# Performance work log

Measured on AMD Instinct MI355X. Metric: run time of the kernel, lower is better.

Reference implementation:

```python
import jax, jax.numpy as jnp
import numpy as np

D_IN = 2048
D_OUT = 2048
H = 16
QK_ROPE = 64
QK_NOPE = 64
QK_HEAD = QK_NOPE + QK_ROPE  # 128
V_HEAD = 128
KV_RANK = 512
THETA = 10000.0
EPS = 1e-6


def rms_norm(x, w):
    var = jnp.mean(x * x, axis=-1, keepdims=True)
    return x * jax.lax.rsqrt(var + EPS) * w


def apply_rope(x, theta=THETA):
    # x: [B, S, H, D] with D even; interleaved-pair rotation (torchtune style)
    B, S, NH, D = x.shape
    half = D // 2
    freqs = 1.0 / (theta ** (jnp.arange(0, D, 2, dtype=jnp.float32) / D))  # [D/2]
    ang = jnp.arange(S, dtype=jnp.float32)[:, None] * freqs[None, :]       # [S, D/2]
    cos = jnp.cos(ang)[None, :, None, :]  # [1,S,1,D/2]
    sin = jnp.sin(ang)[None, :, None, :]
    xp = x.reshape(B, S, NH, half, 2)
    x1, x2 = xp[..., 0], xp[..., 1]
    out = jnp.stack([x1 * cos - x2 * sin, x2 * cos + x1 * sin], axis=-1)
    return out.reshape(B, S, NH, D).astype(x.dtype)


def setup_inputs() -> dict:
    key = jax.random.key(0)
    ks = jax.random.split(key, 6)
    B, S = 2, 2048
    s = lambda fan_in: 1.0 / np.sqrt(fan_in)
    x = jax.random.normal(ks[0], (B, S, D_IN), dtype=jnp.float32)
    w_query = jax.random.uniform(ks[1], (D_IN, H * QK_HEAD), jnp.float32, -s(D_IN), s(D_IN))
    wkv_a = jax.random.uniform(ks[2], (D_IN, KV_RANK + QK_ROPE), jnp.float32, -s(D_IN), s(D_IN))
    wkv_b = jax.random.uniform(ks[3], (KV_RANK, H * (QK_NOPE + V_HEAD)), jnp.float32, -s(KV_RANK), s(KV_RANK))
    kv_norm_w = jnp.ones((KV_RANK,), jnp.float32)
    out_proj_w = jax.random.uniform(ks[4], (H * V_HEAD, D_OUT), jnp.float32, -s(H * V_HEAD), s(H * V_HEAD))
    return {"x": x, "w_query": w_query, "wkv_a": wkv_a, "wkv_b": wkv_b,
            "kv_norm_w": kv_norm_w, "out_proj_w": out_proj_w}


def reference(x, w_query, wkv_a, wkv_b, kv_norm_w, out_proj_w):
    B, S, _ = x.shape
    scale = QK_HEAD ** -0.5
    # queries (no q-lora)
    q = (x @ w_query).reshape(B, S, H, QK_HEAD)
    # low-rank KV compression
    kv = x @ wkv_a                                    # [B,S,KV_RANK+QK_ROPE]
    kv_c, k_pe = kv[..., :KV_RANK], kv[..., KV_RANK:]
    kv_dec = (rms_norm(kv_c, kv_norm_w) @ wkv_b).reshape(B, S, H, QK_NOPE + V_HEAD)
    k_nope, v = kv_dec[..., :QK_NOPE], kv_dec[..., QK_NOPE:]
    k_pe = jnp.broadcast_to(k_pe[:, :, None, :], (B, S, H, QK_ROPE))
    q_nope, q_pe = q[..., :QK_NOPE], q[..., QK_NOPE:]
    q_pe = apply_rope(q_pe)
    k_pe = apply_rope(k_pe)
    queries = jnp.concatenate([q_nope, q_pe], axis=-1)   # [B,S,H,QK_HEAD]
    keys = jnp.concatenate([k_nope, k_pe], axis=-1)
    # attention
    scores = jnp.einsum('bqhd,bkhd->bhqk', queries, keys) * scale
    mask = jnp.triu(jnp.ones((S, S), dtype=bool), k=1)
    scores = jnp.where(mask[None, None], -jnp.inf, scores)
    attn = jax.nn.softmax(scores.astype(jnp.float32), axis=-1).astype(x.dtype)
    out = jnp.einsum('bhqk,bkhd->bqhd', attn, v).reshape(B, S, H * V_HEAD)
    return out @ out_proj_w
```

## Files before the change

### kernel.cpp

```cpp
#include <hip/hip_runtime.h>
#include <hip/hip_bf16.h>
#include <math.h>

#define BATCH   2
#define SEQ     2048
#define D_IN    2048
#define NHEAD   16
#define QK_ROPE 64
#define QK_NOPE 64
#define QK_HEAD 128
#define V_HEAD  128
#define KV_RANK 512
#define KV_W    640
#define NTOK    (BATCH*SEQ)
#define EPS_F   1e-6f

typedef unsigned short u16;
typedef short bf16x8 __attribute__((ext_vector_type(8)));
typedef float f32x4  __attribute__((ext_vector_type(4)));

__device__ __forceinline__ u16 f2bf(float f) {
    unsigned u = __float_as_uint(f);
    return (u16)((u + 0x7fffu + ((u >> 16) & 1u)) >> 16);
}
__device__ __forceinline__ float bf2f(u16 u) {
    return __uint_as_float(((unsigned)u) << 16);
}
__device__ __forceinline__ float exp2_hw(float x) {
    float r;
    asm volatile("v_exp_f32 %0, %1\n\ts_nop 0" : "=v"(r) : "v"(x));
    return r;
}
__device__ __forceinline__ void gload16(const void* g, void* l) {
    __builtin_amdgcn_global_load_lds((const __attribute__((address_space(1))) unsigned int*)g,
                                     (__attribute__((address_space(3))) unsigned int*)l, 16, 0, 0);
}

__device__ __forceinline__ void transpose_sec(const float* __restrict__ src,
                                              u16* __restrict__ dst,
                                              int N, int K, int bx, int by,
                                              float (*tile)[33], int tid) {
    const int tx = tid & 31, ty = tid >> 5;
    const int nb = bx * 32, kb = by * 32;
#pragma unroll
    for (int i = 0; i < 4; ++i) {
        int k = kb + ty + 8 * i, n = nb + tx;
        tile[ty + 8 * i][tx] = (n < N) ? src[(size_t)k * N + n] : 0.f;
    }
    __syncthreads();
#pragma unroll
    for (int i = 0; i < 4; ++i) {
        int n = nb + ty + 8 * i, k = kb + tx;
        dst[(size_t)n * K + k] = f2bf(tile[tx][ty + 8 * i]);
    }
}

__global__ __launch_bounds__(256) void prep(const float* __restrict__ x, u16* __restrict__ x_bf,
                                            const float* __restrict__ wq, u16* __restrict__ wqT,
                                            const float* __restrict__ wkva, u16* __restrict__ wkvaT,
                                            const float* __restrict__ wkvb, u16* __restrict__ wkvbT,
                                            const float* __restrict__ op, u16* __restrict__ opT,
                                            float* __restrict__ tab) {
    __shared__ float tile[32][33];
    const int idx = blockIdx.x;
    const int tid = threadIdx.x;
    if (idx < 8192) {
        int gid = idx * 256 + tid;
        float4 v = ((const float4*)x)[gid];
        unsigned lo = (unsigned)f2bf(v.x) | ((unsigned)f2bf(v.y) << 16);
        unsigned hi = (unsigned)f2bf(v.z) | ((unsigned)f2bf(v.w) << 16);
        ((uint2*)x_bf)[gid] = make_uint2(lo, hi);
    } else if (idx < 12288) {
        int s = idx - 8192;
        transpose_sec(wq, wqT, 2048, 2048, s % 64, s / 64, tile, tid);
    } else if (idx < 13568) {
        int s = idx - 12288;
        transpose_sec(wkva, wkvaT, 576, 2048, s % 20, s / 20, tile, tid);
    } else if (idx < 15104) {
        int s = idx - 13568;
        transpose_sec(wkvb, wkvbT, 3072, 512, s % 96, s / 96, tile, tid);
    } else if (idx < 19200) {
        int s = idx - 15104;
        transpose_sec(op, opT, 2048, 2048, s % 64, s / 64, tile, tid);
    } else {
        int gid = (idx - 19200) * 256 + tid;
        int i = gid & 31, s = gid >> 5;
        float freq = __expf(-(float)(2 * i) / 64.0f * 9.210340371976184f);
        float ang = (float)s * freq;
        tab[2 * gid]     = cosf(ang);
        tab[2 * gid + 1] = sinf(ang);
    }
}

template <int EPI>
__global__ __launch_bounds__(512, 1) void gemm256(const u16* __restrict__ A,
                                                  const u16* __restrict__ BT,
                                                  void* __restrict__ out0,
                                                  void* __restrict__ out1,
                                                  const float* __restrict__ tab,
                                                  int gx, int N, int K, float oscale) {
    __shared__ u16 lds[49152];
    const int tid = threadIdx.x;
    const int w = tid >> 6, l = tid & 63;
    const int lr = l & 15, lg = l >> 4;
    const int wr = w >> 2;
    const int wc = w & 3;
    const int nwg = gridDim.x, q8 = nwg >> 3;
    const int wg = (blockIdx.x & 7) * q8 + (blockIdx.x >> 3);
    const int row0 = (wg / gx) * 256, col0 = (wg % gx) * 256;
    const int NT = K >> 5;

    f32x4 acc[8][4];
#pragma unroll
    for (int m = 0; m < 8; ++m)
#pragma unroll
        for (int n = 0; n < 4; ++n) acc[m][n] = (f32x4){0.f, 0.f, 0.f, 0.f};

    auto stageA = [&](int bufi, int kt) {
        u16* base = lds + bufi * 8192;
        const u16* g = A + (size_t)row0 * K + kt * 32;
#pragma unroll
        for (int i = 0; i < 2; ++i) {
            int L = (i * 512 + tid) * 16;
            int s = L ^ (((L >> 6) & 3) << 4);
            gload16(g + (size_t)(L >> 6) * K + ((s & 63) >> 1), base + (L >> 1));
        }
    };
    auto stageB = [&](int bufi, int kt) {
        u16* base = lds + 24576 + bufi * 8192;
        const u16* g = BT + (size_t)col0 * K + kt * 32;
#pragma unroll
        for (int i = 0; i < 2; ++i) {
            int L = (i * 512 + tid) * 16;
            int s = L ^ (((L >> 6) & 3) << 4);
            gload16(g + (size_t)(L >> 6) * K + ((s & 63) >> 1), base + (L >> 1));
        }
    };

    stageA(0, 0); stageB(0, 0); stageA(1, 1); stageB(1, 1);

    for (int t = 0; t < NT; ++t) {
        const int buf = t % 3, nb2 = (t + 2) % 3;
        u16* Ab = lds + buf * 8192;
        u16* Bb = lds + 24576 + buf * 8192;
        if (t + 1 < NT) asm volatile("s_waitcnt vmcnt(4)" ::: "memory");
        else            asm volatile("s_waitcnt vmcnt(0)" ::: "memory");
        __builtin_amdgcn_s_barrier();
        __builtin_amdgcn_sched_barrier(0);

        bf16x8 bfg[4], af[4];
#pragma unroll
        for (int n = 0; n < 4; ++n) {
            int row = wc * 64 + n * 16 + lr;
            bfg[n] = *(const bf16x8*)&Bb[row * 32 + (((lg * 16) ^ ((row & 3) << 4)) >> 1)];
        }
#pragma unroll
        for (int i = 0; i < 4; ++i) {
            int row = wr * 128 + i * 16 + lr;
            af[i] = *(const bf16x8*)&Ab[row * 32 + (((lg * 16) ^ ((row & 3) << 4)) >> 1)];
        }
        if (t + 2 < NT) stageA(nb2, t + 2);
        __builtin_amdgcn_s_barrier();
        asm volatile("s_waitcnt lgkmcnt(0)" ::: "memory");
        __builtin_amdgcn_sched_barrier(0);
        __builtin_amdgcn_s_setprio(1);
#pragma unroll
        for (int i = 0; i < 4; ++i)
#pragma unroll
            for (int n = 0; n < 4; ++n)
                acc[i][n] = __builtin_amdgcn_mfma_f32_16x16x32_bf16(af[i], bfg[n], acc[i][n], 0, 0, 0);
        __builtin_amdgcn_s_setprio(0);

#pragma unroll
        for (int i = 0; i < 4; ++i) {
            int row = wr * 128 + (4 + i) * 16 + lr;
            af[i] = *(const bf16x8*)&Ab[row * 32 + (((lg * 16) ^ ((row & 3) << 4)) >> 1)];
        }
        if (t + 2 < NT) stageB(nb2, t + 2);
        __builtin_amdgcn_s_barrier();
        asm volatile("s_waitcnt lgkmcnt(0)" ::: "memory");
        __builtin_amdgcn_sched_barrier(0);
        __builtin_amdgcn_s_setprio(1);
#pragma unroll
        for (int i = 0; i < 4; ++i)
#pragma unroll
            for (int n = 0; n < 4; ++n)
                acc[4 + i][n] = __builtin_amdgcn_mfma_f32_16x16x32_bf16(af[i], bfg[n], acc[4 + i][n], 0, 0, 0);
        __builtin_amdgcn_s_setprio(0);
    }

    if (EPI == 0) {
        u16* qp = (u16*)out0;
        float* kvp = (float*)out1;
        const bool pe = (wc & 1);
#pragma unroll
        for (int m = 0; m < 8; ++m)
#pragma unroll
            for (int n = 0; n < 4; ++n) {
                int c = col0 + wc * 64 + n * 16 + lr;
#pragma unroll
                for (int j = 0; j < 4; ++j) {
                    int r = row0 + wr * 128 + m * 16 + 4 * lg + j;
                    float v = acc[m][n][j];
                    if (c < 2048) {
                        v *= oscale;
                        if (pe) {
                            int s = r & (SEQ - 1);
                            int ip = (16 * n + lr) >> 1;
                            float2 cs = ((const float2*)tab)[s * 32 + ip];
                            float part = __shfl_xor(v, 1);
                            v = (lr & 1) ? (v * cs.x + part * cs.y)
                                         : (v * cs.x - part * cs.y);
                        }
                        qp[(size_t)r * 2048 + c] = f2bf(v);
                    } else if (c < 2688) {
                        kvp[(size_t)r * KV_W + (c - 2048)] = v;
                    }
                }
            }
    } else {
        u16* Kall = (u16*)out0;
        u16* Vt   = (u16*)out1;
#pragma unroll
        for (int m = 0; m < 8; ++m) {
            int r0 = row0 + wr * 128 + m * 16 + 4 * lg;
            int b  = r0 >> 11;
            int s0 = r0 & (SEQ - 1);
#pragma unroll
            for (int n = 0; n < 4; ++n) {
                int c = col0 + wc * 64 + n * 16 + lr;
                int h = (unsigned)c / 192u;
                int cr = c - h * 192;
                int bh = b * NHEAD + h;
                if (cr < 64) {
#pragma unroll
                    for (int j = 0; j < 4; ++j) {
                        int s = s0 + j;
                        Kall[((size_t)bh * SEQ + s) * 128 + (cr ^ ((s & 7) << 3))] = f2bf(acc[m][n][j]);
                    }
                } else {
                    int d = cr - 64;
                    union { u16 u[4]; uint2 v; } pk;
#pragma unroll
                    for (int j = 0; j < 4; ++j) pk.u[j] = f2bf(acc[m][n][j]);
                    size_t base = ((size_t)bh * 128 + d) * SEQ + (s0 & ~63);
                    *(uint2*)&Vt[base + ((s0 & 63) ^ ((d & 7) << 3))] = pk.v;
                }
            }
        }
    }
}

__global__ __launch_bounds__(512, 1) void gemm_out(const u16* __restrict__ A,
                                                   const u16* __restrict__ BT,
                                                   float* __restrict__ C,
                                                   int N, int K) {
    __shared__ u16 lds[73728];
    const int tid = threadIdx.x;
    const int w = tid >> 6, l = tid & 63;
    const int lr = l & 15, lg = l >> 4;
    const int wr = w >> 1, wc = w & 1;
    const int nwg = gridDim.x, q8 = nwg >> 3;
    const int wg = (blockIdx.x & 7) * q8 + (blockIdx.x >> 3);
    const int gx = N >> 7;
    const int row0 = (wg / gx) * 256, col0 = (wg % gx) * 128;
    const int NT = K >> 6;

    f32x4 acc[4][4];
#pragma unroll
    for (int m = 0; m < 4; ++m)
#pragma unroll
        for (int n = 0; n < 4; ++n) acc[m][n] = (f32x4){0.f, 0.f, 0.f, 0.f};

    auto stageA = [&](int bufi, int h, int kt) {
        u16* base = lds + bufi * 16384 + h * 8192;
        const u16* g = A + (size_t)(row0 + h * 128) * K + kt * 64;
#pragma unroll
        for (int i = 0; i < 2; ++i) {
            int L = (i * 512 + tid) * 16;
            int s = L ^ (((L >> 7) & 7) << 4);
            gload16(g + (size_t)(s >> 7) * K + ((s & 127) >> 1), base + (L >> 1));
        }
    };
    auto stageB = [&](int bufi, int kt) {
        u16* base = lds + 49152 + bufi * 8192;
        const u16* g = BT + (size_t)col0 * K + kt * 64;
#pragma unroll
        for (int i = 0; i < 2; ++i) {
            int L = (i * 512 + tid) * 16;
            int s = L ^ (((L >> 7) & 7) << 4);
            gload16(g + (size_t)(s >> 7) * K + ((s & 127) >> 1), base + (L >> 1));
        }
    };

    stageA(0, 0, 0); stageA(0, 1, 0); stageB(0, 0);
    stageA(1, 0, 1); stageA(1, 1, 1); stageB(1, 1);

    const int ar0 = (wr & 1) * 64;

    for (int t = 0; t < NT; ++t) {
        const int buf = t % 3, nb2 = (t + 2) % 3;
        u16* Ab = lds + buf * 16384 + (wr >> 1) * 8192;
        u16* Bb = lds + 49152 + buf * 8192;
        if (t + 1 < NT) asm volatile("s_waitcnt vmcnt(6)" ::: "memory");
        else            asm volatile("s_waitcnt vmcnt(0)" ::: "memory");
        __builtin_amdgcn_s_barrier();
        __builtin_amdgcn_sched_barrier(0);

#pragma unroll
        for (int q = 0; q < 2; ++q) {
            bf16x8 af[4], bfg[4];
#pragma unroll
            for (int i = 0; i < 4; ++i) {
                int row = ar0 + i * 16 + lr;
                int byte = row * 128 + q * 64 + lg * 16;
                af[i] = *(const bf16x8*)&Ab[(byte ^ ((row & 7) << 4)) >> 1];
            }
#pragma unroll
            for (int n = 0; n < 4; ++n) {
                int row = wc * 64 + n * 16 + lr;
                int byte = row * 128 + q * 64 + lg * 16;
                bfg[n] = *(const bf16x8*)&Bb[(byte ^ ((row & 7) << 4)) >> 1];
            }
            if (t + 2 < NT) {
                if (q == 0) { stageA(nb2, 0, t + 2); stageA(nb2, 1, t + 2); }
                else        { stageB(nb2, t + 2); }
            }
            __builtin_amdgcn_s_barrier();
            asm volatile("s_waitcnt lgkmcnt(0)" ::: "memory");
            __builtin_amdgcn_sched_barrier(0);
            __builtin_amdgcn_s_setprio(1);
#pragma unroll
            for (int i = 0; i < 4; ++i)
#pragma unroll
                for (int n = 0; n < 4; ++n)
                    acc[i][n] = __builtin_amdgcn_mfma_f32_16x16x32_bf16(
                        af[i], bfg[n], acc[i][n], 0, 0, 0);
            __builtin_amdgcn_s_setprio(0);
        }
    }

#pragma unroll
    for (int m = 0; m < 4; ++m)
#pragma unroll
        for (int n = 0; n < 4; ++n) {
            int c = col0 + wc * 64 + n * 16 + lr;
#pragma unroll
            for (int j = 0; j < 4; ++j) {
                int r = row0 + wr * 64 + m * 16 + 4 * lg + j;
                C[(size_t)r * N + c] = acc[m][n][j];
            }
        }
}

__global__ __launch_bounds__(256) void rmsnorm_bf(const float* __restrict__ kv,
                                                  const float* __restrict__ w,
                                                  u16* __restrict__ c_norm,
                                                  const float* __restrict__ tab,
                                                  u16* __restrict__ K_all) {
    __shared__ float red[256];
    const int row = blockIdx.x, t = threadIdx.x;
    const float* src = kv + (size_t)row * KV_W;
    float v0 = src[t], v1 = src[t + 256];
    red[t] = v0 * v0 + v1 * v1;
    __syncthreads();
    for (int s = 128; s > 0; s >>= 1) {
        if (t < s) red[t] += red[t + s];
        __syncthreads();
    }
    const float inv = rsqrtf(red[0] / (float)KV_RANK + EPS_F);
    u16* dst = c_norm + (size_t)row * KV_RANK;
    dst[t]       = f2bf(v0 * inv * w[t]);
    dst[t + 256] = f2bf(v1 * inv * w[t + 256]);

    if (t < 16) {
        const int dq = t;
        const int s = row & (SEQ - 1);
        const int b = row >> 11;
        float4 v = *(const float4*)(src + KV_RANK + 4 * dq);
        const int i0 = 2 * dq;
        float2 cs0 = ((const float2*)tab)[s * 32 + i0];
        float2 cs1 = ((const float2*)tab)[s * 32 + i0 + 1];
        union { u16 u[4]; uint2 w2; } pk;
        pk.u[0] = f2bf(v.x * cs0.x - v.y * cs0.y);
        pk.u[1] = f2bf(v.y * cs0.x + v.x * cs0.y);
        pk.u[2] = f2bf(v.z * cs1.x - v.w * cs1.y);
        pk.u[3] = f2bf(v.w * cs1.x + v.z * cs1.y);
        const int idx = (64 + 4 * dq) ^ ((s & 7) << 3);
#pragma unroll
        for (int h = 0; h < NHEAD; ++h) {
            int bh = b * NHEAD + h;
            *(uint2*)&K_all[((size_t)bh * SEQ + s) * 128 + idx] = pk.w2;
        }
    }
}

#define QTILE 64
#define KTILE 64

__global__ __launch_bounds__(256, 2) void attn_mfma(const u16* __restrict__ q_bf,
                                                    const u16* __restrict__ K_all,
                                                    const u16* __restrict__ Vt,
                                                    u16* __restrict__ attn_bf) {
    __shared__ u16 Kbuf[2][KTILE * 128];
    __shared__ u16 Vbuf[2][128 * KTILE];
    __shared__ u16 Plds[4][16 * KTILE];

    const int idx = blockIdx.x;
    const int bh = (idx & 7) + 8 * (idx >> 7);
    const int pi = (idx >> 3) & 15;
    const int b = bh >> 4, h = bh & 15;

    const int tid = threadIdx.x;
    const int w = tid >> 6, l = tid & 63;
    const int lr = l & 15, lg = l >> 4;
    const u16* Kb = K_all + (size_t)bh * SEQ * 128;
    const u16* Vb = Vt + (size_t)bh * 128 * SEQ;
    const int sw = (lr & 7) << 3;
    u16* pw = Plds[w];

    auto stage = [&](int bufi, int k0) {
        u16* kb = Kbuf[bufi];
        u16* vb = Vbuf[bufi];
#pragma unroll
        for (int it = 0; it < 4; ++it) {
            int ci = it * 256 + tid;
            gload16(Kb + (((size_t)(k0 + (ci >> 4))) << 7) + ((ci & 15) << 3),
                    kb + (ci << 3));
        }
#pragma unroll
        for (int it = 0; it < 4; ++it) {
            int ci = it * 256 + tid;
            gload16(Vb + (size_t)(ci >> 3) * SEQ + k0 + ((ci & 7) << 3),
                    vb + (ci << 3));
        }
    };

    const int qbA = (31 - pi) * QTILE;
    const int qbB = pi * QTILE;

    stage(0, 0);
    int cur = 0;
    for (int half = 0; half < 2; ++half) {
        const int qbase = half ? qbB : qbA;
        const int nkt = (qbase >> 6) + 1;
        const int qg = qbase + 16 * w + lr;

        const u16* qrow = q_bf + (size_t)(b * SEQ + qg) * 2048 + h * QK_HEAD;
        bf16x8 qf[4];
#pragma unroll
        for (int dc = 0; dc < 4; ++dc) qf[dc] = *(const bf16x8*)(qrow + dc * 32 + lg * 8);

        f32x4 oacc[8];
#pragma unroll
        for (int ft = 0; ft < 8; ++ft) oacc[ft] = (f32x4){0.f, 0.f, 0.f, 0.f};
        float m_r = -1e30f, l_r = 0.f;

        for (int kt = 0; kt < nkt; ++kt) {
            const int k0 = kt * KTILE;
            if (kt + 1 < nkt) {
                stage(cur ^ 1, k0 + KTILE);
                asm volatile("s_waitcnt vmcnt(8)" ::: "memory");
            } else if (half == 0) {
                stage(cur ^ 1, 0);
                asm volatile("s_waitcnt vmcnt(8)" ::: "memory");
            } else {
                asm volatile("s_waitcnt vmcnt(0)" ::: "memory");
            }
            __builtin_amdgcn_s_barrier();
            __builtin_amdgcn_sched_barrier(0);

            const u16* kb = Kbuf[cur];
            const u16* vb = Vbuf[cur];

            f32x4 s[4];
            __builtin_amdgcn_s_setprio(1);
#pragma unroll
            for (int f = 0; f < 4; ++f) {
                s[f] = (f32x4){0.f, 0.f, 0.f, 0.f};
#pragma unroll
                for (int dc = 0; dc < 4; ++dc) {
                    bf16x8 kf = *(const bf16x8*)&kb[(16 * f + lr) * 128 + ((32 * dc + 8 * lg) ^ sw)];
                    s[f] = __builtin_amdgcn_mfma_f32_16x16x32_bf16(kf, qf[dc], s[f], 0, 0, 0);
                }
            }
            __builtin_amdgcn_s_setprio(0);

            if (kt == nkt - 1) {
#pragma unroll
                for (int f = 0; f < 4; ++f)
#pragma unroll
                    for (int j = 0; j < 4; ++j)
                        if (k0 + 16 * f + 4 * lg + j > qg) s[f][j] = -1e30f;
            }

            float t0 = fmaxf(fmaxf(s[0][0], s[0][1]), fmaxf(s[0][2], s[0][3]));
            float t1 = fmaxf(fmaxf(s[1][0], s[1][1]), fmaxf(s[1][2], s[1][3]));
            float t2 = fmaxf(fmaxf(s[2][0], s[2][1]), fmaxf(s[2][2], s[2][3]));
            float t3 = fmaxf(fmaxf(s[3][0], s[3][1]), fmaxf(s[3][2], s[3][3]));
            float t = fmaxf(fmaxf(t0, t1), fmaxf(t2, t3));
            t = fmaxf(t, __shfl_xor(t, 16));
            t = fmaxf(t, __shfl_xor(t, 32));
            bool up = (t > m_r + 11.5f);
            float newm = up ? t : m_r;
            float sf_ = up ? exp2_hw(m_r - t) : 1.0f;
            m_r = newm;
            float rs = 0.f;
#pragma unroll
            for (int f = 0; f < 4; ++f)
#pragma unroll
                for (int j = 0; j < 4; ++j) {
                    float p = exp2_hw(s[f][j] - newm);
                    s[f][j] = p;
                    rs += p;
                }
            rs += __shfl_xor(rs, 16);
            rs += __shfl_xor(rs, 32);
            l_r = l_r * sf_ + rs;
            if (__any(up)) {
#pragma unroll
                for (int ft = 0; ft < 8; ++ft)
#pragma unroll
                    for (int j = 0; j < 4; ++j) oacc[ft][j] *= sf_;
            }

#pragma unroll
            for (int f = 0; f < 4; ++f) {
                union { u16 u[4]; uint2 v; } pk;
#pragma unroll
                for (int j = 0; j < 4; ++j) pk.u[j] = f2bf(s[f][j]);
                *(uint2*)&pw[lr * 64 + ((16 * f + 4 * lg) ^ sw)] = pk.v;
            }
            asm volatile("s_waitcnt lgkmcnt(0)" ::: "memory");
            bf16x8 pfr[2];
#pragma unroll
            for (int ks = 0; ks < 2; ++ks)
                pfr[ks] = *(const bf16x8*)&pw[lr * 64 + ((32 * ks + 8 * lg) ^ sw)];

            __builtin_amdgcn_s_setprio(1);
#pragma unroll
            for (int ft = 0; ft < 8; ++ft) {
                int d = 16 * ft + lr;
#pragma unroll
                for (int ks = 0; ks < 2; ++ks) {
                    bf16x8 vf = *(const bf16x8*)&vb[d * 64 + ((32 * ks + 8 * lg) ^ sw)];
                    oacc[ft] = __builtin_amdgcn_mfma_f32_16x16x32_bf16(vf, pfr[ks], oacc[ft], 0, 0, 0);
                }
            }
            __builtin_amdgcn_s_setprio(0);

            __builtin_amdgcn_s_barrier();
            cur ^= 1;
        }

        const float inv = 1.0f / l_r;
        u16* orow = attn_bf + (size_t)(b * SEQ + qg) * 2048 + h * V_HEAD;
#pragma unroll
        for (int ft = 0; ft < 8; ++ft) {
            union { u16 u[4]; uint2 v; } ok;
#pragma unroll
            for (int j = 0; j < 4; ++j) ok.u[j] = f2bf(oacc[ft][j] * inv);
            *(uint2*)(orow + 16 * ft + 4 * lg) = ok.v;
        }
    }
}

extern "C" void kernel_launch(void* const* d_in, const int* in_sizes, int n_in,
                              void* d_out, int out_size, void* d_ws, size_t ws_size,
                              hipStream_t stream) {
    const float* x         = (const float*)d_in[0];
    const float* w_query   = (const float*)d_in[1];
    const float* wkv_a     = (const float*)d_in[2];
    const float* wkv_b     = (const float*)d_in[3];
    const float* kv_norm_w = (const float*)d_in[4];
    const float* out_proj  = (const float*)d_in[5];

    u16* x_bf     = (u16*)d_ws;
    u16* q_bf     = x_bf + (size_t)8388608;
    u16* c_norm   = q_bf + (size_t)8388608;
    u16* kvdec_bf = c_norm + (size_t)2097152;
    u16* K_all    = kvdec_bf + (size_t)12582912;
    u16* Vt       = K_all + (size_t)8388608;
    u16* wT       = Vt + (size_t)8388608;
    u16* wkvaT    = wT + (size_t)4194304;
    u16* wkvbT    = wkvaT + (size_t)1310720;
    u16* opT      = wkvbT + (size_t)1572864;
    float* kv     = (float*)(opT + (size_t)4194304);
    float* tab    = kv + (size_t)2621440;
    u16* attn_bf  = x_bf;
    float* out = (float*)d_out;

    const float qscale2 = 0.08838834764831845f * 1.4426950408889634f;

    prep<<<19456, 256, 0, stream>>>(x, x_bf, w_query, wT, wkv_a, wkvaT,
                                    wkv_b, wkvbT, out_proj, opT, tab);

    gemm256<0><<<176, 512, 0, stream>>>(x_bf, wT, q_bf, kv, tab,
                                        11, 2688, 2048, qscale2);
    rmsnorm_bf<<<NTOK, 256, 0, stream>>>(kv, kv_norm_w, c_norm, tab, K_all);
    gemm256<2><<<192, 512, 0, stream>>>(c_norm, wkvbT, K_all, Vt, nullptr,
                                        12, 3072, 512, 1.0f);

    attn_mfma<<<512, 256, 0, stream>>>(q_bf, K_all, Vt, attn_bf);

    gemm_out<<<256, 512, 0, stream>>>(attn_bf, opT, out, 2048, 2048);
}
```

Baseline: 246.5 us.

## Replace 256x256 GEMMs with unified 128x128 multi-occupancy GEMM kernel

Shrinks the projection GEMM tile from 256x256 (512 threads, one block per CU) to 128x128 (256 threads, up to three blocks per CU) and uses a new XOR swizzle for LDS. The separate out-projection GEMM is folded into the same template as a plain float-store epilogue. The aim is better CU fill (672/768/512 blocks instead of 176/192/256) and latency hiding through occupancy. In exchange, smaller tiles halve per-block operand reuse, which raises global/L2 traffic, and each K step now has a single barrier.

```diff
diff --git a/kernel.cpp b/kernel.cpp
--- a/kernel.cpp
+++ b/kernel.cpp
@@ -93,46 +93,47 @@
 }
 
 template <int EPI>
-__global__ __launch_bounds__(512, 1) void gemm256(const u16* __restrict__ A,
+__global__ __launch_bounds__(256, 3) void gemm128(const u16* __restrict__ A,
                                                   const u16* __restrict__ BT,
                                                   void* __restrict__ out0,
                                                   void* __restrict__ out1,
                                                   const float* __restrict__ tab,
                                                   int gx, int N, int K, float oscale) {
-    __shared__ u16 lds[49152];
+    __shared__ u16 lds[24576];
     const int tid = threadIdx.x;
     const int w = tid >> 6, l = tid & 63;
     const int lr = l & 15, lg = l >> 4;
-    const int wr = w >> 2;
-    const int wc = w & 3;
+    const int wr = w >> 1, wc = w & 1;
     const int nwg = gridDim.x, q8 = nwg >> 3;
     const int wg = (blockIdx.x & 7) * q8 + (blockIdx.x >> 3);
-    const int row0 = (wg / gx) * 256, col0 = (wg % gx) * 256;
+    const int row0 = (wg / gx) * 128, col0 = (wg % gx) * 128;
     const int NT = K >> 5;
 
-    f32x4 acc[8][4];
-#pragma unroll
-    for (int m = 0; m < 8; ++m)
+    f32x4 acc[4][4];
+#pragma unroll
+    for (int m = 0; m < 4; ++m)
 #pragma unroll
         for (int n = 0; n < 4; ++n) acc[m][n] = (f32x4){0.f, 0.f, 0.f, 0.f};
 
     auto stageA = [&](int bufi, int kt) {
-        u16* base = lds + bufi * 8192;
+        u16* base = lds + bufi * 4096;
         const u16* g = A + (size_t)row0 * K + kt * 32;
 #pragma unroll
         for (int i = 0; i < 2; ++i) {
-            int L = (i * 512 + tid) * 16;
-            int s = L ^ (((L >> 6) & 3) << 4);
+            int L = (i * 256 + tid) * 16;
+            int f = ((L >> 6) ^ (L >> 8)) & 3;
+            int s = L ^ (f << 4);
             gload16(g + (size_t)(L >> 6) * K + ((s & 63) >> 1), base + (L >> 1));
         }
     };
     auto stageB = [&](int bufi, int kt) {
-        u16* base = lds + 24576 + bufi * 8192;
+        u16* base = lds + 12288 + bufi * 4096;
         const u16* g = BT + (size_t)col0 * K + kt * 32;
 #pragma unroll
         for (int i = 0; i < 2; ++i) {
-            int L = (i * 512 + tid) * 16;
-            int s = L ^ (((L >> 6) & 3) << 4);
+            int L = (i * 256 + tid) * 16;
+            int f = ((L >> 6) ^ (L >> 8)) & 3;
+            int s = L ^ (f << 4);
             gload16(g + (size_t)(L >> 6) * K + ((s & 63) >> 1), base + (L >> 1));
         }
     };
@@ -141,26 +142,27 @@
 
     for (int t = 0; t < NT; ++t) {
         const int buf = t % 3, nb2 = (t + 2) % 3;
-        u16* Ab = lds + buf * 8192;
-        u16* Bb = lds + 24576 + buf * 8192;
+        u16* Ab = lds + buf * 4096;
+        u16* Bb = lds + 12288 + buf * 4096;
         if (t + 1 < NT) asm volatile("s_waitcnt vmcnt(4)" ::: "memory");
         else            asm volatile("s_waitcnt vmcnt(0)" ::: "memory");
         __builtin_amdgcn_s_barrier();
         __builtin_amdgcn_sched_barrier(0);
 
-        bf16x8 bfg[4], af[4];
+        bf16x8 af[4], bfg[4];
 #pragma unroll
         for (int n = 0; n < 4; ++n) {
             int row = wc * 64 + n * 16 + lr;
-            bfg[n] = *(const bf16x8*)&Bb[row * 32 + (((lg * 16) ^ ((row & 3) << 4)) >> 1)];
+            int fr = (row ^ (row >> 2)) & 3;
+            bfg[n] = *(const bf16x8*)&Bb[(row * 64 + ((lg ^ fr) << 4)) >> 1];
         }
 #pragma unroll
         for (int i = 0; i < 4; ++i) {
-            int row = wr * 128 + i * 16 + lr;
-            af[i] = *(const bf16x8*)&Ab[row * 32 + (((lg * 16) ^ ((row & 3) << 4)) >> 1)];
-        }
-        if (t + 2 < NT) stageA(nb2, t + 2);
-        __builtin_amdgcn_s_barrier();
+            int row = wr * 64 + i * 16 + lr;
+            int fr = (row ^ (row >> 2)) & 3;
+            af[i] = *(const bf16x8*)&Ab[(row * 64 + ((lg ^ fr) << 4)) >> 1];
+        }
+        if (t + 2 < NT) { stageA(nb2, t + 2); stageB(nb2, t + 2); }
         asm volatile("s_waitcnt lgkmcnt(0)" ::: "memory");
         __builtin_amdgcn_sched_barrier(0);
         __builtin_amdgcn_s_setprio(1);
@@ -170,37 +172,20 @@
             for (int n = 0; n < 4; ++n)
                 acc[i][n] = __builtin_amdgcn_mfma_f32_16x16x32_bf16(af[i], bfg[n], acc[i][n], 0, 0, 0);
         __builtin_amdgcn_s_setprio(0);
-
-#pragma unroll
-        for (int i = 0; i < 4; ++i) {
-            int row = wr * 128 + (4 + i) * 16 + lr;
-            af[i] = *(const bf16x8*)&Ab[row * 32 + (((lg * 16) ^ ((row & 3) << 4)) >> 1)];
-        }
-        if (t + 2 < NT) stageB(nb2, t + 2);
-        __builtin_amdgcn_s_barrier();
-        asm volatile("s_waitcnt lgkmcnt(0)" ::: "memory");
-        __builtin_amdgcn_sched_barrier(0);
-        __builtin_amdgcn_s_setprio(1);
-#pragma unroll
-        for (int i = 0; i < 4; ++i)
-#pragma unroll
-            for (int n = 0; n < 4; ++n)
-                acc[4 + i][n] = __builtin_amdgcn_mfma_f32_16x16x32_bf16(af[i], bfg[n], acc[4 + i][n], 0, 0, 0);
-        __builtin_amdgcn_s_setprio(0);
     }
 
     if (EPI == 0) {
         u16* qp = (u16*)out0;
         float* kvp = (float*)out1;
-        const bool pe = (wc & 1);
-#pragma unroll
-        for (int m = 0; m < 8; ++m)
+        const bool pe = (wc == 1);
+#pragma unroll
+        for (int m = 0; m < 4; ++m)
 #pragma unroll
             for (int n = 0; n < 4; ++n) {
                 int c = col0 + wc * 64 + n * 16 + lr;
 #pragma unroll
                 for (int j = 0; j < 4; ++j) {
-                    int r = row0 + wr * 128 + m * 16 + 4 * lg + j;
+                    int r = row0 + wr * 64 + m * 16 + 4 * lg + j;
                     float v = acc[m][n][j];
                     if (c < 2048) {
                         v *= oscale;
@@ -213,17 +198,30 @@
                                          : (v * cs.x - part * cs.y);
                         }
                         qp[(size_t)r * 2048 + c] = f2bf(v);
-                    } else if (c < 2688) {
+                    } else {
                         kvp[(size_t)r * KV_W + (c - 2048)] = v;
                     }
                 }
             }
+    } else if (EPI == 1) {
+        float* C = (float*)out0;
+#pragma unroll
+        for (int m = 0; m < 4; ++m)
+#pragma unroll
+            for (int n = 0; n < 4; ++n) {
+                int c = col0 + wc * 64 + n * 16 + lr;
+#pragma unroll
+                for (int j = 0; j < 4; ++j) {
+                    int r = row0 + wr * 64 + m * 16 + 4 * lg + j;
+                    C[(size_t)r * N + c] = acc[m][n][j];
+                }
+            }
     } else {
         u16* Kall = (u16*)out0;
         u16* Vt   = (u16*)out1;
 #pragma unroll
-        for (int m = 0; m < 8; ++m) {
-            int r0 = row0 + wr * 128 + m * 16 + 4 * lg;
+        for (int m = 0; m < 4; ++m) {
+            int r0 = row0 + wr * 64 + m * 16 + 4 * lg;
             int b  = r0 >> 11;
             int s0 = r0 & (SEQ - 1);
 #pragma unroll
@@ -249,108 +247,6 @@
             }
         }
     }
-}
-
-__global__ __launch_bounds__(512, 1) void gemm_out(const u16* __restrict__ A,
-                                                   const u16* __restrict__ BT,
-                                                   float* __restrict__ C,
-                                                   int N, int K) {
-    __shared__ u16 lds[73728];
-    const int tid = threadIdx.x;
-    const int w = tid >> 6, l = tid & 63;
-    const int lr = l & 15, lg = l >> 4;
-    const int wr = w >> 1, wc = w & 1;
-    const int nwg = gridDim.x, q8 = nwg >> 3;
-    const int wg = (blockIdx.x & 7) * q8 + (blockIdx.x >> 3);
-    const int gx = N >> 7;
-    const int row0 = (wg / gx) * 256, col0 = (wg % gx) * 128;
-    const int NT = K >> 6;
-
-    f32x4 acc[4][4];
-#pragma unroll
-    for (int m = 0; m < 4; ++m)
-#pragma unroll
-        for (int n = 0; n < 4; ++n) acc[m][n] = (f32x4){0.f, 0.f, 0.f, 0.f};
-
-    auto stageA = [&](int bufi, int h, int kt) {
-        u16* base = lds + bufi * 16384 + h * 8192;
-        const u16* g = A + (size_t)(row0 + h * 128) * K + kt * 64;
-#pragma unroll
-        for (int i = 0; i < 2; ++i) {
-            int L = (i * 512 + tid) * 16;
-            int s = L ^ (((L >> 7) & 7) << 4);
-            gload16(g + (size_t)(s >> 7) * K + ((s & 127) >> 1), base + (L >> 1));
-        }
-    };
-    auto stageB = [&](int bufi, int kt) {
-        u16* base = lds + 49152 + bufi * 8192;
-        const u16* g = BT + (size_t)col0 * K + kt * 64;
-#pragma unroll
-        for (int i = 0; i < 2; ++i) {
-            int L = (i * 512 + tid) * 16;
-            int s = L ^ (((L >> 7) & 7) << 4);
-            gload16(g + (size_t)(s >> 7) * K + ((s & 127) >> 1), base + (L >> 1));
-        }
-    };
-
-    stageA(0, 0, 0); stageA(0, 1, 0); stageB(0, 0);
-    stageA(1, 0, 1); stageA(1, 1, 1); stageB(1, 1);
-
-    const int ar0 = (wr & 1) * 64;
-
-    for (int t = 0; t < NT; ++t) {
-        const int buf = t % 3, nb2 = (t + 2) % 3;
-        u16* Ab = lds + buf * 16384 + (wr >> 1) * 8192;
-        u16* Bb = lds + 49152 + buf * 8192;
-        if (t + 1 < NT) asm volatile("s_waitcnt vmcnt(6)" ::: "memory");
-        else            asm volatile("s_waitcnt vmcnt(0)" ::: "memory");
-        __builtin_amdgcn_s_barrier();
-        __builtin_amdgcn_sched_barrier(0);
-
-#pragma unroll
-        for (int q = 0; q < 2; ++q) {
-            bf16x8 af[4], bfg[4];
-#pragma unroll
-            for (int i = 0; i < 4; ++i) {
-                int row = ar0 + i * 16 + lr;
-                int byte = row * 128 + q * 64 + lg * 16;
-                af[i] = *(const bf16x8*)&Ab[(byte ^ ((row & 7) << 4)) >> 1];
-            }
-#pragma unroll
-            for (int n = 0; n < 4; ++n) {
-                int row = wc * 64 + n * 16 + lr;
-                int byte = row * 128 + q * 64 + lg * 16;
-                bfg[n] = *(const bf16x8*)&Bb[(byte ^ ((row & 7) << 4)) >> 1];
-            }
-            if (t + 2 < NT) {
-                if (q == 0) { stageA(nb2, 0, t + 2); stageA(nb2, 1, t + 2); }
-                else        { stageB(nb2, t + 2); }
-            }
-            __builtin_amdgcn_s_barrier();
-            asm volatile("s_waitcnt lgkmcnt(0)" ::: "memory");
-            __builtin_amdgcn_sched_barrier(0);
-            __builtin_amdgcn_s_setprio(1);
-#pragma unroll
-            for (int i = 0; i < 4; ++i)
-#pragma unroll
-                for (int n = 0; n < 4; ++n)
-                    acc[i][n] = __builtin_amdgcn_mfma_f32_16x16x32_bf16(
-                        af[i], bfg[n], acc[i][n], 0, 0, 0);
-            __builtin_amdgcn_s_setprio(0);
-        }
-    }
-
-#pragma unroll
-    for (int m = 0; m < 4; ++m)
-#pragma unroll
-        for (int n = 0; n < 4; ++n) {
-            int c = col0 + wc * 64 + n * 16 + lr;
-#pragma unroll
-            for (int j = 0; j < 4; ++j) {
-                int r = row0 + wr * 64 + m * 16 + 4 * lg + j;
-                C[(size_t)r * N + c] = acc[m][n][j];
-            }
-        }
 }
 
 __global__ __launch_bounds__(256) void rmsnorm_bf(const float* __restrict__ kv,
@@ -595,13 +491,14 @@
     prep<<<19456, 256, 0, stream>>>(x, x_bf, w_query, wT, wkv_a, wkvaT,
                                     wkv_b, wkvbT, out_proj, opT, tab);
 
-    gemm256<0><<<176, 512, 0, stream>>>(x_bf, wT, q_bf, kv, tab,
-                                        11, 2688, 2048, qscale2);
+    gemm128<0><<<672, 256, 0, stream>>>(x_bf, wT, q_bf, kv, tab,
+                                        21, 2688, 2048, qscale2);
     rmsnorm_bf<<<NTOK, 256, 0, stream>>>(kv, kv_norm_w, c_norm, tab, K_all);
-    gemm256<2><<<192, 512, 0, stream>>>(c_norm, wkvbT, K_all, Vt, nullptr,
-                                        12, 3072, 512, 1.0f);
+    gemm128<2><<<768, 256, 0, stream>>>(c_norm, wkvbT, K_all, Vt, nullptr,
+                                        24, 3072, 512, 1.0f);
 
     attn_mfma<<<512, 256, 0, stream>>>(q_bf, K_all, Vt, attn_bf);
 
-    gemm_out<<<256, 512, 0, stream>>>(attn_bf, opT, out, 2048, 2048);
-}
+    gemm128<1><<<512, 256, 0, stream>>>(attn_bf, opT, out, nullptr, nullptr,
+                                        16, 2048, 2048, 1.0f);
+}
```

After: 228.4 us. -7.4%, faster.
